# Performance work log

Hardware: AMD Instinct MI355X
Metric: run time of the kernel (lower is better)

## Reference

```python
import jax, jax.numpy as jnp
import numpy as np

B, T, D = 32, 512, 64   # batch, timesteps, latent dim
H, S = 64, 4096         # hidden_size, state_dim
EPS = 1e-6              # flax LayerNorm default epsilon


def _glorot(k, shape):
    lim = np.sqrt(6.0 / (shape[0] + shape[1])).astype(np.float32)
    return jax.random.uniform(k, shape, jnp.float32, -lim, lim)


def setup_inputs() -> dict:
    key = jax.random.key(0)
    ks = jax.random.split(key, 7)
    # gate order in the fused 4H axis: i, f, g, o ; flax inits f-gate bias to 1
    bh = jnp.concatenate([jnp.zeros((H,)), jnp.ones((H,)), jnp.zeros((2 * H,))]).astype(jnp.float32)
    return {
        "enc_outputs": jax.random.normal(ks[0], (B, T, D), jnp.float32),
        "Wx": _glorot(ks[1], (D, 4 * H)),   # input->gates, no bias (flax dense_i)
        "Wh": _glorot(ks[2], (H, 4 * H)),   # hidden->gates
        "bh": bh,
        "W1": _glorot(ks[3], (H, 2 * H)), "b1": jnp.zeros((2 * H,), jnp.float32),
        "g1": jnp.ones((2 * H,), jnp.float32), "be1": jnp.zeros((2 * H,), jnp.float32),
        "W2": _glorot(ks[4], (2 * H, 2 * H)), "b2": jnp.zeros((2 * H,), jnp.float32),
        "g2": jnp.ones((2 * H,), jnp.float32), "be2": jnp.zeros((2 * H,), jnp.float32),
        "Wo": _glorot(ks[5], (2 * H, S)), "bo": jnp.zeros((S,), jnp.float32),
    }


def _layernorm(x, g, b):
    m = x.mean(-1, keepdims=True)
    v = ((x - m) ** 2).mean(-1, keepdims=True)
    return (x - m) * jax.lax.rsqrt(v + EPS) * g + b


def _lstm(enc, Wx, Wh, bh):
    # precompute all input projections in one big GEMM: [B,T,4H]
    xg = jnp.einsum('btd,dg->btg', enc, Wx)

    def step(carry, x_t):
        c, h = carry
        z = x_t + h @ Wh + bh              # [B,4H]
        i, f, g, o = jnp.split(z, 4, axis=-1)
        c = jax.nn.sigmoid(f) * c + jax.nn.sigmoid(i) * jnp.tanh(g)
        h = jax.nn.sigmoid(o) * jnp.tanh(c)
        return (c, h), h

    b = enc.shape[0]
    init = (jnp.zeros((b, H), enc.dtype), jnp.zeros((b, H), enc.dtype))
    _, hs = jax.lax.scan(step, init, xg.swapaxes(0, 1))  # hs: [T,B,H]
    return hs.swapaxes(0, 1)                              # [B,T,H]


def reference(enc_outputs, Wx, Wh, bh, W1, b1, g1, be1, W2, b2, g2, be2, Wo, bo):
    b, t, _ = enc_outputs.shape
    dec = _lstm(enc_outputs, Wx, Wh, bh)            # [B,T,H]
    flat = dec.reshape(b * t, H)
    h = jax.nn.gelu(_layernorm(flat @ W1 + b1, g1, be1))   # flax gelu: tanh approx
    # dropout deterministic (train=False) -> identity
    h = jax.nn.gelu(_layernorm(h @ W2 + b2, g2, be2))
    out = h @ Wo + bo                                # [B*T,S]
    return out.reshape(b, t, S)
```

## Files before the change

### kernel.cpp

```cpp
#include <hip/hip_runtime.h>
#include <hip/hip_bf16.h>

#define T_ 512

typedef __attribute__((ext_vector_type(8))) short short8;
typedef __attribute__((ext_vector_type(4))) float f32x4;

__device__ __forceinline__ float fast_rcp(float x){ return __builtin_amdgcn_rcpf(x); }
__device__ __forceinline__ float sigmoid_f(float x){
  return fast_rcp(1.f + __expf(-x));
}
__device__ __forceinline__ float tanh_f(float x){
  return fmaf(2.f, fast_rcp(1.f + __expf(-2.f*x)), -1.f);
}
__device__ __forceinline__ float gelu_f(float x){
  float u = 0.7978845608028654f*(x + 0.044715f*x*x*x);
  return 0.5f*x*(1.f + tanh_f(u));
}
__device__ __forceinline__ unsigned short bf16_bits(float x){
  __hip_bfloat16 b = __float2bfloat16(x);
  return __builtin_bit_cast(unsigned short, b);
}
__device__ __forceinline__ float bits_f32(unsigned short u){
  return __uint_as_float(((unsigned)u) << 16);
}
__device__ __forceinline__ void bar_lds(){
  asm volatile("s_waitcnt lgkmcnt(0)\n\ts_barrier" ::: "memory");
}

__global__ __launch_bounds__(256) void k_encT(const float* __restrict__ enc,
                                              unsigned short* __restrict__ encB)
{
  int i = blockIdx.x*256 + threadIdx.x;
  int b = i >> 15, t = (i >> 6) & 511, d = i & 63;
  float v = enc[i];
  unsigned short hi = bf16_bits(v);
  float rem = v - bits_f32(hi);
  unsigned short lo = bf16_bits(rem);
  size_t o = (size_t)t*4096 + b*128 + d;
  encB[o]      = hi;
  encB[o + 64] = lo;
}

__global__ __launch_bounds__(256) void k_whxT(const float* __restrict__ Wh,
                                              const float* __restrict__ Wx,
                                              unsigned short* __restrict__ WhxT)
{
  int i = blockIdx.x*256 + threadIdx.x;
  int j = i >> 7, k = i & 127;
  float v = (k < 64) ? Wh[k*256 + j] : Wx[(k - 64)*256 + j];
  WhxT[i] = bf16_bits(v);
}

__global__ __launch_bounds__(256, 1) void k_lstm(const unsigned short* __restrict__ encB,
                                                 const unsigned short* __restrict__ WhxT,
                                                 const float* __restrict__ bh,
                                                 unsigned short* __restrict__ hsb)
{
  __shared__ __align__(16) unsigned short Hb[2][16][72];
  int tid = threadIdx.x;
  int w = tid >> 6, l = tid & 63;
  int m = l & 15, q = l >> 4;
  int mb = m & 7;
  bool hi = (m >= 8);
  int bo = blockIdx.x * 8;
  int col0 = 16*w + 4*q;

  const short* Wr = (const short*)WhxT;
  short8 ah[4][2], ax[4][2];
#pragma unroll
  for (int g = 0; g < 4; ++g)
#pragma unroll
    for (int kk = 0; kk < 2; ++kk){
      ah[g][kk] = *(const short8*)(Wr + (64*g + 16*w + m)*128 +      kk*32 + q*8);
      ax[g][kk] = *(const short8*)(Wr + (64*g + 16*w + m)*128 + 64 + kk*32 + q*8);
    }
  f32x4 bb[4];
#pragma unroll
  for (int g = 0; g < 4; ++g){
    bb[g][0] = bh[64*g + 16*w + 4*q + 0];
    bb[g][1] = bh[64*g + 16*w + 4*q + 1];
    bb[g][2] = bh[64*g + 16*w + 4*q + 2];
    bb[g][3] = bh[64*g + 16*w + 4*q + 3];
  }

  for (int i = tid; i < 1152; i += 256) ((unsigned int*)&Hb[0][0][0])[i] = 0;

  const unsigned short* encp = encB;
  int em = (bo + mb)*128;
  unsigned short* hsrow = hsb + ((size_t)(bo + mb)*512)*64 + col0 + (hi ? 2 : 0);

  short8 EA0,EA1,EA2,EA3, EB0,EB1,EB2,EB3, EC0,EC1,EC2,EC3, ED0,ED1,ED2,ED3;
  short8 e0,e1,e2,e3;
  e0 = *(const short8*)(encp + 0*4096 + em      + q*8);
  e1 = *(const short8*)(encp + 0*4096 + em + 32 + q*8);
  e2 = *(const short8*)(encp + 0*4096 + em + 64 + q*8);
  e3 = *(const short8*)(encp + 0*4096 + em + 96 + q*8);
  EB0 = *(const short8*)(encp + 1*4096 + em      + q*8);
  EB1 = *(const short8*)(encp + 1*4096 + em + 32 + q*8);
  EB2 = *(const short8*)(encp + 1*4096 + em + 64 + q*8);
  EB3 = *(const short8*)(encp + 1*4096 + em + 96 + q*8);
  EC0 = *(const short8*)(encp + 2*4096 + em      + q*8);
  EC1 = *(const short8*)(encp + 2*4096 + em + 32 + q*8);
  EC2 = *(const short8*)(encp + 2*4096 + em + 64 + q*8);
  EC3 = *(const short8*)(encp + 2*4096 + em + 96 + q*8);
  ED0 = *(const short8*)(encp + 3*4096 + em      + q*8);
  ED1 = *(const short8*)(encp + 3*4096 + em + 32 + q*8);
  ED2 = *(const short8*)(encp + 3*4096 + em + 64 + q*8);
  ED3 = *(const short8*)(encp + 3*4096 + em + 96 + q*8);

  f32x4 xacc[4];
#pragma unroll
  for (int g = 0; g < 4; ++g){
    f32x4 a = __builtin_amdgcn_mfma_f32_16x16x32_bf16(ax[g][0], e0, bb[g], 0,0,0);
    a = __builtin_amdgcn_mfma_f32_16x16x32_bf16(ax[g][1], e1, a, 0,0,0);
    a = __builtin_amdgcn_mfma_f32_16x16x32_bf16(ax[g][0], e2, a, 0,0,0);
    xacc[g] = __builtin_amdgcn_mfma_f32_16x16x32_bf16(ax[g][1], e3, a, 0,0,0);
  }
  float c0 = 0.f, c1 = 0.f;
  __syncthreads();

#define STEP(tt, EU0,EU1,EU2,EU3, EL0,EL1,EL2,EL3)                             \
  {                                                                            \
    const unsigned short* hb = &Hb[(tt) & 1][0][0];                            \
    short8 hv0 = *(const short8*)(hb + m*72 +      q*8);                       \
    short8 hv1 = *(const short8*)(hb + m*72 + 32 + q*8);                       \
    {                     \
      const unsigned short* ep = encp + (size_t)((tt)+4)*4096 + em;            \
      EL0 = *(const short8*)(ep +      q*8);                                   \
      EL1 = *(const short8*)(ep + 32 + q*8);                                   \
      EL2 = *(const short8*)(ep + 64 + q*8);                                   \
      EL3 = *(const short8*)(ep + 96 + q*8);                                   \
    }                                                                          \
    f32x4 z0 = __builtin_amdgcn_mfma_f32_16x16x32_bf16(ah[0][0], hv0, xacc[0], 0,0,0); \
    f32x4 z1 = __builtin_amdgcn_mfma_f32_16x16x32_bf16(ah[1][0], hv0, xacc[1], 0,0,0); \
    f32x4 z2 = __builtin_amdgcn_mfma_f32_16x16x32_bf16(ah[2][0], hv0, xacc[2], 0,0,0); \
    f32x4 z3 = __builtin_amdgcn_mfma_f32_16x16x32_bf16(ah[3][0], hv0, xacc[3], 0,0,0); \
    z0 = __builtin_amdgcn_mfma_f32_16x16x32_bf16(ah[0][1], hv1, z0, 0,0,0);    \
    z1 = __builtin_amdgcn_mfma_f32_16x16x32_bf16(ah[1][1], hv1, z1, 0,0,0);    \
    z2 = __builtin_amdgcn_mfma_f32_16x16x32_bf16(ah[2][1], hv1, z2, 0,0,0);    \
    z3 = __builtin_amdgcn_mfma_f32_16x16x32_bf16(ah[3][1], hv1, z3, 0,0,0);    \
       \
    float i2 = __shfl_xor(z0[2], 8), i3 = __shfl_xor(z0[3], 8);                \
    float f2 = __shfl_xor(z1[2], 8), f3 = __shfl_xor(z1[3], 8);                \
    float g2 = __shfl_xor(z2[2], 8), g3 = __shfl_xor(z2[3], 8);                \
    float o2 = __shfl_xor(z3[2], 8), o3 = __shfl_xor(z3[3], 8);                \
    float zia = hi ? i2 : z0[0], zib = hi ? i3 : z0[1];                        \
    float zfa = hi ? f2 : z1[0], zfb = hi ? f3 : z1[1];                        \
    float zga = hi ? g2 : z2[0], zgb = hi ? g3 : z2[1];                        \
    float zoa = hi ? o2 : z3[0], zob = hi ? o3 : z3[1];                        \
    float h0, h1;                                                              \
    { float si=sigmoid_f(zia), sf=sigmoid_f(zfa);                              \
      float tg=tanh_f(zga),    so=sigmoid_f(zoa);                              \
      c0 = sf*c0 + si*tg; h0 = so*tanh_f(c0); }                                \
    { float si=sigmoid_f(zib), sf=sigmoid_f(zfb);                              \
      float tg=tanh_f(zgb),    so=sigmoid_f(zob);                              \
      c1 = sf*c1 + si*tg; h1 = so*tanh_f(c1); }                                \
    ushort2 hp;                                                                \
    hp.x = bf16_bits(h0); hp.y = bf16_bits(h1);                                \
    *(ushort2*)(&Hb[((tt)+1) & 1][mb][col0 + (hi ? 2 : 0)]) = hp;              \
    *(ushort2*)(hsrow + (size_t)(tt)*64) = hp;                                 \
    xacc[0] = __builtin_amdgcn_mfma_f32_16x16x32_bf16(ax[0][0], EU0, bb[0], 0,0,0); \
    xacc[1] = __builtin_amdgcn_mfma_f32_16x16x32_bf16(ax[1][0], EU0, bb[1], 0,0,0); \
    xacc[2] = __builtin_amdgcn_mfma_f32_16x16x32_bf16(ax[2][0], EU0, bb[2], 0,0,0); \
    xacc[3] = __builtin_amdgcn_mfma_f32_16x16x32_bf16(ax[3][0], EU0, bb[3], 0,0,0); \
    xacc[0] = __builtin_amdgcn_mfma_f32_16x16x32_bf16(ax[0][1], EU1, xacc[0], 0,0,0); \
    xacc[1] = __builtin_amdgcn_mfma_f32_16x16x32_bf16(ax[1][1], EU1, xacc[1], 0,0,0); \
    xacc[2] = __builtin_amdgcn_mfma_f32_16x16x32_bf16(ax[2][1], EU1, xacc[2], 0,0,0); \
    xacc[3] = __builtin_amdgcn_mfma_f32_16x16x32_bf16(ax[3][1], EU1, xacc[3], 0,0,0); \
    xacc[0] = __builtin_amdgcn_mfma_f32_16x16x32_bf16(ax[0][0], EU2, xacc[0], 0,0,0); \
    xacc[1] = __builtin_amdgcn_mfma_f32_16x16x32_bf16(ax[1][0], EU2, xacc[1], 0,0,0); \
    xacc[2] = __builtin_amdgcn_mfma_f32_16x16x32_bf16(ax[2][0], EU2, xacc[2], 0,0,0); \
    xacc[3] = __builtin_amdgcn_mfma_f32_16x16x32_bf16(ax[3][0], EU2, xacc[3], 0,0,0); \
    xacc[0] = __builtin_amdgcn_mfma_f32_16x16x32_bf16(ax[0][1], EU3, xacc[0], 0,0,0); \
    xacc[1] = __builtin_amdgcn_mfma_f32_16x16x32_bf16(ax[1][1], EU3, xacc[1], 0,0,0); \
    xacc[2] = __builtin_amdgcn_mfma_f32_16x16x32_bf16(ax[2][1], EU3, xacc[2], 0,0,0); \
    xacc[3] = __builtin_amdgcn_mfma_f32_16x16x32_bf16(ax[3][1], EU3, xacc[3], 0,0,0); \
    bar_lds();                                                                 \
  }

  for (int t = 0; t < T_; t += 4){
    STEP(t,   EB0,EB1,EB2,EB3, EA0,EA1,EA2,EA3);
    STEP(t+1, EC0,EC1,EC2,EC3, EB0,EB1,EB2,EB3);
    STEP(t+2, ED0,ED1,ED2,ED3, EC0,EC1,EC2,EC3);
    STEP(t+3, EA0,EA1,EA2,EA3, ED0,ED1,ED2,ED3);
  }
#undef STEP
}

__global__ __launch_bounds__(256) void k_mlp(const unsigned short* __restrict__ hsb,
    const float* __restrict__ W1, const float* __restrict__ b1,
    const float* __restrict__ g1, const float* __restrict__ be1,
    const float* __restrict__ W2, const float* __restrict__ b2,
    const float* __restrict__ g2, const float* __restrict__ be2,
    __hip_bfloat16* __restrict__ h2g)
{
  __shared__ __align__(16) float xs[2][64];
  __shared__ __align__(16) float vs[2][128];
  __shared__ float red[2][2][2];
  int tid = threadIdx.x;
  int jj = tid & 127, rg = tid >> 7;
  int lane = tid & 63;
  int whalf = (tid >> 6) & 1;
  float w1c[64], w2c[128];
#pragma unroll
  for (int k = 0; k < 64; ++k) w1c[k] = W1[k*128 + jj];
#pragma unroll
  for (int k = 0; k < 128; ++k) w2c[k] = W2[k*128 + jj];
  float b1j = b1[jj], g1j = g1[jj], be1j = be1[jj];
  float b2j = b2[jj], g2j = g2[jj], be2j = be2[jj];
  int base = blockIdx.x * 64;
  for (int p = 0; p < 32; ++p){
    int r = base + p*2 + rg;
    if (whalf == 0) xs[rg][lane] = bits_f32(hsb[(size_t)r*64 + lane]);
    __syncthreads();
    float a0 = b1j, a1 = 0.f;
    const float4* x4 = (const float4*)xs[rg];
#pragma unroll
    for (int k4 = 0; k4 < 16; ++k4){
      float4 v = x4[k4];
      a0 = fmaf(v.x, w1c[4*k4+0], a0);
      a1 = fmaf(v.y, w1c[4*k4+1], a1);
      a0 = fmaf(v.z, w1c[4*k4+2], a0);
      a1 = fmaf(v.w, w1c[4*k4+3], a1);
    }
    float a = a0 + a1;
    float s1 = a, s2 = a*a;
#pragma unroll
    for (int off = 32; off > 0; off >>= 1){
      s1 += __shfl_xor(s1, off, 64);
      s2 += __shfl_xor(s2, off, 64);
    }
    if (lane == 0){ red[rg][whalf][0] = s1; red[rg][whalf][1] = s2; }
    __syncthreads();
    s1 = red[rg][0][0] + red[rg][1][0];
    s2 = red[rg][0][1] + red[rg][1][1];
    float mean = s1*(1.f/128.f);
    float var  = s2*(1.f/128.f) - mean*mean;
    float rstd = rsqrtf(var + 1e-6f);
    float y = gelu_f((a - mean)*rstd*g1j + be1j);
    vs[rg][jj] = y;
    __syncthreads();
    float c0 = b2j, c1 = 0.f;
    const float4* v4 = (const float4*)vs[rg];
#pragma unroll
    for (int k4 = 0; k4 < 32; ++k4){
      float4 v = v4[k4];
      c0 = fmaf(v.x, w2c[4*k4+0], c0);
      c1 = fmaf(v.y, w2c[4*k4+1], c1);
      c0 = fmaf(v.z, w2c[4*k4+2], c0);
      c1 = fmaf(v.w, w2c[4*k4+3], c1);
    }
    float cc = c0 + c1;
    float t1 = cc, t2 = cc*cc;
#pragma unroll
    for (int off = 32; off > 0; off >>= 1){
      t1 += __shfl_xor(t1, off, 64);
      t2 += __shfl_xor(t2, off, 64);
    }
    if (lane == 0){ red[rg][whalf][0] = t1; red[rg][whalf][1] = t2; }
    __syncthreads();
    t1 = red[rg][0][0] + red[rg][1][0];
    t2 = red[rg][0][1] + red[rg][1][1];
    mean = t1*(1.f/128.f);
    var  = t2*(1.f/128.f) - mean*mean;
    rstd = rsqrtf(var + 1e-6f);
    float z = gelu_f((cc - mean)*rstd*g2j + be2j);
    h2g[(size_t)r*128 + jj] = __float2bfloat16(z);
  }
}

__global__ __launch_bounds__(256) void k_wot(const float* __restrict__ Wo,
                                             __hip_bfloat16* __restrict__ WoT)
{
  __shared__ __hip_bfloat16 tl[64][130];
  int tid = threadIdx.x;
  int n0 = blockIdx.x * 64;
  for (int idx = tid; idx < 64*128; idx += 256){
    int k = idx >> 6, nl = idx & 63;
    tl[nl][k] = __float2bfloat16(Wo[(size_t)k*4096 + n0 + nl]);
  }
  __syncthreads();
  for (int idx = tid; idx < 64*128; idx += 256){
    int nl = idx >> 7, k = idx & 127;
    WoT[(size_t)(n0 + nl)*128 + k] = tl[nl][k];
  }
}

__global__ __launch_bounds__(256) void k_out(const __hip_bfloat16* __restrict__ h2g,
                                             const __hip_bfloat16* __restrict__ WoT,
                                             const float* __restrict__ bo,
                                             float* __restrict__ out)
{
  int bid0 = blockIdx.x;
  int bid = (bid0 & 7)*512 + (bid0 >> 3);
  int Mb = bid >> 5, Nb = bid & 31;
  int tid = threadIdx.x;
  int w = tid >> 6, l = tid & 63;
  int wm = w >> 1, wn = w & 1;
  int m0 = Mb*128 + wm*64, n0 = Nb*128 + wn*64;
  int lr = l & 15, lk = (l >> 4)*8;
  f32x4 acc[4][4] = {};
  const short* A  = (const short*)WoT;
  const short* Bp = (const short*)h2g;
#pragma unroll
  for (int kk = 0; kk < 4; ++kk){
    int ko = kk*32 + lk;
    short8 av[4], bv[4];
#pragma unroll
    for (int i = 0; i < 4; ++i) av[i] = *(const short8*)(A  + (size_t)(n0 + i*16 + lr)*128 + ko);
#pragma unroll
    for (int i = 0; i < 4; ++i) bv[i] = *(const short8*)(Bp + (size_t)(m0 + i*16 + lr)*128 + ko);
#pragma unroll
    for (int fm = 0; fm < 4; ++fm)
#pragma unroll
      for (int fn = 0; fn < 4; ++fn)
        acc[fm][fn] = __builtin_amdgcn_mfma_f32_16x16x32_bf16(av[fn], bv[fm], acc[fm][fn], 0, 0, 0);
  }
  int nb_ = (l >> 4)*4;
#pragma unroll
  for (int fn = 0; fn < 4; ++fn){
    f32x4 bia = *(const f32x4*)(bo + n0 + fn*16 + nb_);
#pragma unroll
    for (int fm = 0; fm < 4; ++fm){
      size_t row = (size_t)(m0 + fm*16 + lr)*4096;
      __builtin_nontemporal_store(acc[fm][fn] + bia, (f32x4*)(out + row + n0 + fn*16 + nb_));
    }
  }
}

extern "C" void kernel_launch(void* const* d_in, const int* in_sizes, int n_in,
                              void* d_out, int out_size, void* d_ws, size_t ws_size,
                              hipStream_t stream)
{
  const float* enc = (const float*)d_in[0];
  const float* Wx  = (const float*)d_in[1];
  const float* Wh  = (const float*)d_in[2];
  const float* bh  = (const float*)d_in[3];
  const float* W1  = (const float*)d_in[4];
  const float* b1  = (const float*)d_in[5];
  const float* g1  = (const float*)d_in[6];
  const float* be1 = (const float*)d_in[7];
  const float* W2  = (const float*)d_in[8];
  const float* b2  = (const float*)d_in[9];
  const float* g2  = (const float*)d_in[10];
  const float* be2 = (const float*)d_in[11];
  const float* Wo  = (const float*)d_in[12];
  const float* bo  = (const float*)d_in[13];
  float* out = (float*)d_out;

  const size_t encB_bytes = (size_t)(512+4)*4096*2;
  const size_t whx_bytes  = (size_t)256*128*2;
  const size_t hs_bytes   = (size_t)16384*64*2;
  const size_t h2_bytes   = (size_t)16384*128*2;
  const size_t wt_bytes   = (size_t)4096*128*2;
  char* ws = (char*)d_ws;
  unsigned short *encB, *WhxT, *hsb; __hip_bfloat16 *h2g, *WoT;
  if (ws_size >= encB_bytes + whx_bytes + hs_bytes + h2_bytes + wt_bytes){
    encB = (unsigned short*)ws;
    WhxT = (unsigned short*)(ws + encB_bytes);
    hsb  = (unsigned short*)(ws + encB_bytes + whx_bytes);
    h2g  = (__hip_bfloat16*)(ws + encB_bytes + whx_bytes + hs_bytes);
    WoT  = (__hip_bfloat16*)(ws + encB_bytes + whx_bytes + hs_bytes + h2_bytes);
  } else {
    encB = (unsigned short*)d_out;
    WhxT = (unsigned short*)((char*)d_out + encB_bytes);
    hsb  = (unsigned short*)((char*)d_out + encB_bytes + whx_bytes);
    h2g  = (__hip_bfloat16*)ws;
    WoT  = (__hip_bfloat16*)(ws + h2_bytes);
  }

  k_encT<<<4096, 256, 0, stream>>>(enc, encB);
  k_whxT<<<128,  256, 0, stream>>>(Wh, Wx, WhxT);
  k_wot <<<64,   256, 0, stream>>>(Wo, WoT);
  k_lstm<<<4,    256, 0, stream>>>(encB, WhxT, bh, hsb);
  k_mlp <<<256,  256, 0, stream>>>(hsb, W1, b1, g1, be1, W2, b2, g2, be2, h2g);
  k_out <<<4096, 256, 0, stream>>>(h2g, WoT, bo, out);
}
```

Baseline: 465.2 us.

## Split LSTM block into producer and consumer warps for input projections

The LSTM kernel now runs 512 threads per block. Four producer waves compute the input-projection gates (Wx·x + bias) two steps ahead and write them into a 4-slot LDS ring. Four consumer waves read those gates, do the recurrent h·Wh MFMAs and the gate nonlinearities, so the input MFMAs leave the serial critical path. This costs 64KB of LDS and a block-wide barrier every step, and the workspace now reserves room for 8 extra timesteps of encoded input.

```diff
diff --git a/kernel.cpp b/kernel.cpp
--- a/kernel.cpp
+++ b/kernel.cpp
@@ -52,102 +52,109 @@
   WhxT[i] = bf16_bits(v);
 }
 
-__global__ __launch_bounds__(256, 1) void k_lstm(const unsigned short* __restrict__ encB,
+__global__ __launch_bounds__(512, 2) void k_lstm(const unsigned short* __restrict__ encB,
                                                  const unsigned short* __restrict__ WhxT,
                                                  const float* __restrict__ bh,
                                                  unsigned short* __restrict__ hsb)
 {
   __shared__ __align__(16) unsigned short Hb[2][16][72];
+  __shared__ __align__(16) float xsl[4*4*4*256];
   int tid = threadIdx.x;
   int w = tid >> 6, l = tid & 63;
+  bool cons = (w < 4);
+  int wt = w & 3;
   int m = l & 15, q = l >> 4;
   int mb = m & 7;
   bool hi = (m >= 8);
   int bo = blockIdx.x * 8;
-  int col0 = 16*w + 4*q;
+  int col0 = 16*wt + 4*q;
 
   const short* Wr = (const short*)WhxT;
   short8 ah[4][2], ax[4][2];
-#pragma unroll
-  for (int g = 0; g < 4; ++g)
-#pragma unroll
-    for (int kk = 0; kk < 2; ++kk){
-      ah[g][kk] = *(const short8*)(Wr + (64*g + 16*w + m)*128 +      kk*32 + q*8);
-      ax[g][kk] = *(const short8*)(Wr + (64*g + 16*w + m)*128 + 64 + kk*32 + q*8);
-    }
   f32x4 bb[4];
-#pragma unroll
-  for (int g = 0; g < 4; ++g){
-    bb[g][0] = bh[64*g + 16*w + 4*q + 0];
-    bb[g][1] = bh[64*g + 16*w + 4*q + 1];
-    bb[g][2] = bh[64*g + 16*w + 4*q + 2];
-    bb[g][3] = bh[64*g + 16*w + 4*q + 3];
-  }
-
-  for (int i = tid; i < 1152; i += 256) ((unsigned int*)&Hb[0][0][0])[i] = 0;
+  if (cons){
+#pragma unroll
+    for (int g = 0; g < 4; ++g)
+#pragma unroll
+      for (int kk = 0; kk < 2; ++kk)
+        ah[g][kk] = *(const short8*)(Wr + (64*g + 16*wt + m)*128 + kk*32 + q*8);
+  } else {
+#pragma unroll
+    for (int g = 0; g < 4; ++g)
+#pragma unroll
+      for (int kk = 0; kk < 2; ++kk)
+        ax[g][kk] = *(const short8*)(Wr + (64*g + 16*wt + m)*128 + 64 + kk*32 + q*8);
+#pragma unroll
+    for (int g = 0; g < 4; ++g){
+      bb[g][0] = bh[64*g + 16*wt + 4*q + 0];
+      bb[g][1] = bh[64*g + 16*wt + 4*q + 1];
+      bb[g][2] = bh[64*g + 16*wt + 4*q + 2];
+      bb[g][3] = bh[64*g + 16*wt + 4*q + 3];
+    }
+  }
+
+  for (int i = tid; i < 1152; i += 512) ((unsigned int*)&Hb[0][0][0])[i] = 0;
 
   const unsigned short* encp = encB;
   int em = (bo + mb)*128;
   unsigned short* hsrow = hsb + ((size_t)(bo + mb)*512)*64 + col0 + (hi ? 2 : 0);
 
-  short8 EA0,EA1,EA2,EA3, EB0,EB1,EB2,EB3, EC0,EC1,EC2,EC3, ED0,ED1,ED2,ED3;
-  short8 e0,e1,e2,e3;
-  e0 = *(const short8*)(encp + 0*4096 + em      + q*8);
-  e1 = *(const short8*)(encp + 0*4096 + em + 32 + q*8);
-  e2 = *(const short8*)(encp + 0*4096 + em + 64 + q*8);
-  e3 = *(const short8*)(encp + 0*4096 + em + 96 + q*8);
-  EB0 = *(const short8*)(encp + 1*4096 + em      + q*8);
-  EB1 = *(const short8*)(encp + 1*4096 + em + 32 + q*8);
-  EB2 = *(const short8*)(encp + 1*4096 + em + 64 + q*8);
-  EB3 = *(const short8*)(encp + 1*4096 + em + 96 + q*8);
-  EC0 = *(const short8*)(encp + 2*4096 + em      + q*8);
-  EC1 = *(const short8*)(encp + 2*4096 + em + 32 + q*8);
-  EC2 = *(const short8*)(encp + 2*4096 + em + 64 + q*8);
-  EC3 = *(const short8*)(encp + 2*4096 + em + 96 + q*8);
-  ED0 = *(const short8*)(encp + 3*4096 + em      + q*8);
-  ED1 = *(const short8*)(encp + 3*4096 + em + 32 + q*8);
-  ED2 = *(const short8*)(encp + 3*4096 + em + 64 + q*8);
-  ED3 = *(const short8*)(encp + 3*4096 + em + 96 + q*8);
-
-  f32x4 xacc[4];
-#pragma unroll
-  for (int g = 0; g < 4; ++g){
-    f32x4 a = __builtin_amdgcn_mfma_f32_16x16x32_bf16(ax[g][0], e0, bb[g], 0,0,0);
-    a = __builtin_amdgcn_mfma_f32_16x16x32_bf16(ax[g][1], e1, a, 0,0,0);
-    a = __builtin_amdgcn_mfma_f32_16x16x32_bf16(ax[g][0], e2, a, 0,0,0);
-    xacc[g] = __builtin_amdgcn_mfma_f32_16x16x32_bf16(ax[g][1], e3, a, 0,0,0);
-  }
   float c0 = 0.f, c1 = 0.f;
+  short8 EA0,EA1,EA2,EA3, EB0,EB1,EB2,EB3;
+
+  if (!cons){
+#pragma unroll
+    for (int s = 0; s < 2; ++s){
+      const unsigned short* ep = encp + (size_t)s*4096 + em;
+      short8 e0 = *(const short8*)(ep      + q*8);
+      short8 e1 = *(const short8*)(ep + 32 + q*8);
+      short8 e2 = *(const short8*)(ep + 64 + q*8);
+      short8 e3 = *(const short8*)(ep + 96 + q*8);
+#pragma unroll
+      for (int g = 0; g < 4; ++g){
+        f32x4 a = __builtin_amdgcn_mfma_f32_16x16x32_bf16(ax[g][0], e0, bb[g], 0,0,0);
+        a = __builtin_amdgcn_mfma_f32_16x16x32_bf16(ax[g][1], e1, a, 0,0,0);
+        a = __builtin_amdgcn_mfma_f32_16x16x32_bf16(ax[g][0], e2, a, 0,0,0);
+        a = __builtin_amdgcn_mfma_f32_16x16x32_bf16(ax[g][1], e3, a, 0,0,0);
+        *(f32x4*)(xsl + ((s*4 + wt)*4 + g)*256 + l*4) = a;
+      }
+    }
+    EA0 = *(const short8*)(encp + (size_t)2*4096 + em      + q*8);
+    EA1 = *(const short8*)(encp + (size_t)2*4096 + em + 32 + q*8);
+    EA2 = *(const short8*)(encp + (size_t)2*4096 + em + 64 + q*8);
+    EA3 = *(const short8*)(encp + (size_t)2*4096 + em + 96 + q*8);
+    EB0 = *(const short8*)(encp + (size_t)3*4096 + em      + q*8);
+    EB1 = *(const short8*)(encp + (size_t)3*4096 + em + 32 + q*8);
+    EB2 = *(const short8*)(encp + (size_t)3*4096 + em + 64 + q*8);
+    EB3 = *(const short8*)(encp + (size_t)3*4096 + em + 96 + q*8);
+  }
   __syncthreads();
 
-#define STEP(tt, EU0,EU1,EU2,EU3, EL0,EL1,EL2,EL3)                             \
+#define CONS_STEP(tt)                                                          \
   {                                                                            \
     const unsigned short* hb = &Hb[(tt) & 1][0][0];                            \
     short8 hv0 = *(const short8*)(hb + m*72 +      q*8);                       \
     short8 hv1 = *(const short8*)(hb + m*72 + 32 + q*8);                       \
-    {                     \
-      const unsigned short* ep = encp + (size_t)((tt)+4)*4096 + em;            \
-      EL0 = *(const short8*)(ep +      q*8);                                   \
-      EL1 = *(const short8*)(ep + 32 + q*8);                                   \
-      EL2 = *(const short8*)(ep + 64 + q*8);                                   \
-      EL3 = *(const short8*)(ep + 96 + q*8);                                   \
-    }                                                                          \
-    f32x4 z0 = __builtin_amdgcn_mfma_f32_16x16x32_bf16(ah[0][0], hv0, xacc[0], 0,0,0); \
-    f32x4 z1 = __builtin_amdgcn_mfma_f32_16x16x32_bf16(ah[1][0], hv0, xacc[1], 0,0,0); \
-    f32x4 z2 = __builtin_amdgcn_mfma_f32_16x16x32_bf16(ah[2][0], hv0, xacc[2], 0,0,0); \
-    f32x4 z3 = __builtin_amdgcn_mfma_f32_16x16x32_bf16(ah[3][0], hv0, xacc[3], 0,0,0); \
+    const float* xp = xsl + (((tt) & 3)*4 + wt)*4*256 + l*4;                   \
+    f32x4 X0 = *(const f32x4*)(xp        );                                    \
+    f32x4 X1 = *(const f32x4*)(xp +  256 );                                    \
+    f32x4 X2 = *(const f32x4*)(xp +  512 );                                    \
+    f32x4 X3 = *(const f32x4*)(xp +  768 );                                    \
+    f32x4 z0 = __builtin_amdgcn_mfma_f32_16x16x32_bf16(ah[0][0], hv0, X0, 0,0,0); \
+    f32x4 z1 = __builtin_amdgcn_mfma_f32_16x16x32_bf16(ah[1][0], hv0, X1, 0,0,0); \
+    f32x4 z2 = __builtin_amdgcn_mfma_f32_16x16x32_bf16(ah[2][0], hv0, X2, 0,0,0); \
+    f32x4 z3 = __builtin_amdgcn_mfma_f32_16x16x32_bf16(ah[3][0], hv0, X3, 0,0,0); \
     z0 = __builtin_amdgcn_mfma_f32_16x16x32_bf16(ah[0][1], hv1, z0, 0,0,0);    \
     z1 = __builtin_amdgcn_mfma_f32_16x16x32_bf16(ah[1][1], hv1, z1, 0,0,0);    \
     z2 = __builtin_amdgcn_mfma_f32_16x16x32_bf16(ah[2][1], hv1, z2, 0,0,0);    \
     z3 = __builtin_amdgcn_mfma_f32_16x16x32_bf16(ah[3][1], hv1, z3, 0,0,0);    \
-       \
     float i2 = __shfl_xor(z0[2], 8), i3 = __shfl_xor(z0[3], 8);                \
     float f2 = __shfl_xor(z1[2], 8), f3 = __shfl_xor(z1[3], 8);                \
-    float g2 = __shfl_xor(z2[2], 8), g3 = __shfl_xor(z2[3], 8);                \
+    float g2v = __shfl_xor(z2[2], 8), g3 = __shfl_xor(z2[3], 8);               \
     float o2 = __shfl_xor(z3[2], 8), o3 = __shfl_xor(z3[3], 8);                \
     float zia = hi ? i2 : z0[0], zib = hi ? i3 : z0[1];                        \
     float zfa = hi ? f2 : z1[0], zfb = hi ? f3 : z1[1];                        \
-    float zga = hi ? g2 : z2[0], zgb = hi ? g3 : z2[1];                        \
+    float zga = hi ? g2v : z2[0], zgb = hi ? g3 : z2[1];                       \
     float zoa = hi ? o2 : z3[0], zob = hi ? o3 : z3[1];                        \
     float h0, h1;                                                              \
     { float si=sigmoid_f(zia), sf=sigmoid_f(zfa);                              \
@@ -160,32 +167,40 @@
     hp.x = bf16_bits(h0); hp.y = bf16_bits(h1);                                \
     *(ushort2*)(&Hb[((tt)+1) & 1][mb][col0 + (hi ? 2 : 0)]) = hp;              \
     *(ushort2*)(hsrow + (size_t)(tt)*64) = hp;                                 \
-    xacc[0] = __builtin_amdgcn_mfma_f32_16x16x32_bf16(ax[0][0], EU0, bb[0], 0,0,0); \
-    xacc[1] = __builtin_amdgcn_mfma_f32_16x16x32_bf16(ax[1][0], EU0, bb[1], 0,0,0); \
-    xacc[2] = __builtin_amdgcn_mfma_f32_16x16x32_bf16(ax[2][0], EU0, bb[2], 0,0,0); \
-    xacc[3] = __builtin_amdgcn_mfma_f32_16x16x32_bf16(ax[3][0], EU0, bb[3], 0,0,0); \
-    xacc[0] = __builtin_amdgcn_mfma_f32_16x16x32_bf16(ax[0][1], EU1, xacc[0], 0,0,0); \
-    xacc[1] = __builtin_amdgcn_mfma_f32_16x16x32_bf16(ax[1][1], EU1, xacc[1], 0,0,0); \
-    xacc[2] = __builtin_amdgcn_mfma_f32_16x16x32_bf16(ax[2][1], EU1, xacc[2], 0,0,0); \
-    xacc[3] = __builtin_amdgcn_mfma_f32_16x16x32_bf16(ax[3][1], EU1, xacc[3], 0,0,0); \
-    xacc[0] = __builtin_amdgcn_mfma_f32_16x16x32_bf16(ax[0][0], EU2, xacc[0], 0,0,0); \
-    xacc[1] = __builtin_amdgcn_mfma_f32_16x16x32_bf16(ax[1][0], EU2, xacc[1], 0,0,0); \
-    xacc[2] = __builtin_amdgcn_mfma_f32_16x16x32_bf16(ax[2][0], EU2, xacc[2], 0,0,0); \
-    xacc[3] = __builtin_amdgcn_mfma_f32_16x16x32_bf16(ax[3][0], EU2, xacc[3], 0,0,0); \
-    xacc[0] = __builtin_amdgcn_mfma_f32_16x16x32_bf16(ax[0][1], EU3, xacc[0], 0,0,0); \
-    xacc[1] = __builtin_amdgcn_mfma_f32_16x16x32_bf16(ax[1][1], EU3, xacc[1], 0,0,0); \
-    xacc[2] = __builtin_amdgcn_mfma_f32_16x16x32_bf16(ax[2][1], EU3, xacc[2], 0,0,0); \
-    xacc[3] = __builtin_amdgcn_mfma_f32_16x16x32_bf16(ax[3][1], EU3, xacc[3], 0,0,0); \
-    bar_lds();                                                                 \
-  }
-
-  for (int t = 0; t < T_; t += 4){
-    STEP(t,   EB0,EB1,EB2,EB3, EA0,EA1,EA2,EA3);
-    STEP(t+1, EC0,EC1,EC2,EC3, EB0,EB1,EB2,EB3);
-    STEP(t+2, ED0,ED1,ED2,ED3, EC0,EC1,EC2,EC3);
-    STEP(t+3, EA0,EA1,EA2,EA3, ED0,ED1,ED2,ED3);
-  }
-#undef STEP
+  }
+
+#define PROD_STEP(tt, E0,E1,E2,E3)                                             \
+  {                                                                            \
+    f32x4 xa[4];                                                               \
+    _Pragma("unroll")                                                          \
+    for (int g = 0; g < 4; ++g){                                               \
+      f32x4 a = __builtin_amdgcn_mfma_f32_16x16x32_bf16(ax[g][0], E0, bb[g], 0,0,0); \
+      a = __builtin_amdgcn_mfma_f32_16x16x32_bf16(ax[g][1], E1, a, 0,0,0);     \
+      a = __builtin_amdgcn_mfma_f32_16x16x32_bf16(ax[g][0], E2, a, 0,0,0);     \
+      xa[g] = __builtin_amdgcn_mfma_f32_16x16x32_bf16(ax[g][1], E3, a, 0,0,0); \
+    }                                                                          \
+    float* xp = xsl + ((((tt)+2) & 3)*4 + wt)*4*256 + l*4;                     \
+    *(f32x4*)(xp       ) = xa[0];                                              \
+    *(f32x4*)(xp +  256) = xa[1];                                              \
+    *(f32x4*)(xp +  512) = xa[2];                                              \
+    *(f32x4*)(xp +  768) = xa[3];                                              \
+    const unsigned short* ep = encp + (size_t)((tt)+4)*4096 + em;              \
+    E0 = *(const short8*)(ep      + q*8);                                      \
+    E1 = *(const short8*)(ep + 32 + q*8);                                      \
+    E2 = *(const short8*)(ep + 64 + q*8);                                      \
+    E3 = *(const short8*)(ep + 96 + q*8);                                      \
+  }
+
+  for (int t = 0; t < T_; t += 2){
+    if (cons) CONS_STEP(t)
+    else      PROD_STEP(t, EA0,EA1,EA2,EA3)
+    bar_lds();
+    if (cons) CONS_STEP(t+1)
+    else      PROD_STEP(t+1, EB0,EB1,EB2,EB3)
+    bar_lds();
+  }
+#undef CONS_STEP
+#undef PROD_STEP
 }
 
 __global__ __launch_bounds__(256) void k_mlp(const unsigned short* __restrict__ hsb,
@@ -349,7 +364,7 @@
   const float* bo  = (const float*)d_in[13];
   float* out = (float*)d_out;
 
-  const size_t encB_bytes = (size_t)(512+4)*4096*2;
+  const size_t encB_bytes = (size_t)(512+8)*4096*2;
   const size_t whx_bytes  = (size_t)256*128*2;
   const size_t hs_bytes   = (size_t)16384*64*2;
   const size_t h2_bytes   = (size_t)16384*128*2;
@@ -373,7 +388,7 @@
   k_encT<<<4096, 256, 0, stream>>>(enc, encB);
   k_whxT<<<128,  256, 0, stream>>>(Wh, Wx, WhxT);
   k_wot <<<64,   256, 0, stream>>>(Wo, WoT);
-  k_lstm<<<4,    256, 0, stream>>>(encB, WhxT, bh, hsb);
+  k_lstm<<<4,    512, 0, stream>>>(encB, WhxT, bh, hsb);
   k_mlp <<<256,  256, 0, stream>>>(hsb, W1, b1, g1, be1, W2, b2, g2, be2, h2g);
   k_out <<<4096, 256, 0, stream>>>(h2g, WoT, bo, out);
 }
```

Result: no change. 456.2 us (-1.9%).
